# Kernel optimization log

Measured on AMD Instinct MI355X. Metric: run time of the kernel, lower is better.

Reference implementation:

```python
import jax, jax.numpy as jnp
import numpy as np

N = 100000   # nodes
E = 3200000  # random edges (before self-loops)
D = 20       # hidden width


def setup_inputs() -> dict:
    key = jax.random.key(0)
    k = jax.random.split(key, 8)
    return {
        "feat": jax.random.normal(k[0], (N, 1), jnp.float32),
        "W_start": jax.random.normal(k[1], (1, D), jnp.float32) * 0.5,
        "b_start": jnp.zeros((D,), jnp.float32),
        "W_mid": jax.random.normal(k[2], (18, D, D), jnp.float32) * (1.0 / np.sqrt(D)),
        "b_mid": jnp.zeros((18, D), jnp.float32),
        "W_final": jax.random.normal(k[3], (D, D), jnp.float32) * (1.0 / np.sqrt(D)),
        "b_final": jnp.zeros((D,), jnp.float32),
        "src": jax.random.randint(k[4], (E,), 0, N, jnp.int32),
        "dst": jax.random.randint(k[5], (E,), 0, N, jnp.int32),
    }


def reference(feat, W_start, b_start, W_mid, b_mid, W_final, b_final, src, dst):
    # dgl.add_self_loop
    loop = jnp.arange(N, dtype=src.dtype)
    src2 = jnp.concatenate([src, loop])
    dst2 = jnp.concatenate([dst, loop])

    ones = jnp.ones(src2.shape[0], jnp.float32)
    out_deg = jax.ops.segment_sum(ones, src2, num_segments=N)
    in_deg = jax.ops.segment_sum(ones, dst2, num_segments=N)
    # with self-loops degrees >= 1; clamp defensively like DGL
    dout = jnp.power(jnp.maximum(out_deg, 1.0), -0.5)  # [N]
    din = jnp.power(jnp.maximum(in_deg, 1.0), -0.5)    # [N]

    def conv(h, W, b):
        # GraphConv norm='both': D_out^{-1/2} on source, sum-aggregate, D_in^{-1/2} on dest
        hw = (h * dout[:, None]) @ W                   # [N, out]
        agg = jax.ops.segment_sum(hw[src2], dst2, num_segments=N)
        return agg * din[:, None] + b

    h = jax.nn.relu(conv(feat, W_start, b_start))

    def step(h, wb):
        W, b = wb
        return jax.nn.relu(conv(h, W, b)), None

    h, _ = jax.lax.scan(step, h, (W_mid, b_mid))
    h = conv(h, W_final, b_final)
    return h[None]  # unsqueeze(0) -> [1, N, D]
```

## Files before the change

kernel.cpp:

```cpp
#include <hip/hip_runtime.h>

#define DH    20
#define BKSC  10
#define BKC   1024
#define MAXKC 128
#define MAXNB 512
#define BKSF  8
#define BKF   256
#define ECAP  10240
#define CHUNK 8192


__global__ void zero_bhist2(int* __restrict__ bhist_d, int* __restrict__ bhist_s) {
    int i = threadIdx.x;
    if (i < MAXKC) { bhist_d[i] = 0; bhist_s[i] = 0; }
}

__global__ __launch_bounds__(256) void bucket_hist2(const int* __restrict__ src,
        const int* __restrict__ dst, int* __restrict__ pbh_d,
        int* __restrict__ pbh_s, int* __restrict__ bhist_d,
        int* __restrict__ bhist_s, int E, int K) {
    __shared__ int hd[MAXKC];
    __shared__ int hs[MAXKC];
    for (int i = threadIdx.x; i < K; i += blockDim.x) { hd[i] = 0; hs[i] = 0; }
    __syncthreads();
    int lo = blockIdx.x * CHUNK;
    int hi = lo + CHUNK; if (hi > E) hi = E;
    for (int e = lo + (int)threadIdx.x; e < hi; e += 256) {
        atomicAdd(&hd[__builtin_nontemporal_load(&dst[e]) >> BKSC], 1);
        atomicAdd(&hs[__builtin_nontemporal_load(&src[e]) >> BKSC], 1);
    }
    __syncthreads();
    for (int i = threadIdx.x; i < K; i += blockDim.x) {
        pbh_d[blockIdx.x * MAXKC + i] = hd[i];
        pbh_s[blockIdx.x * MAXKC + i] = hs[i];
        if (hd[i]) atomicAdd(&bhist_d[i], hd[i]);
        if (hs[i]) atomicAdd(&bhist_s[i], hs[i]);
    }
}

__global__ __launch_bounds__(128) void bucket_scan2(
        const int* __restrict__ bhist_d, int* __restrict__ bbase_d,
        int* __restrict__ bcursor_d, const int* __restrict__ bhist_s,
        int* __restrict__ bbase_s, int* __restrict__ bcursor_s, int K) {
    __shared__ int a[MAXKC];
    __shared__ int b[MAXKC];
    int t = threadIdx.x;
    int vd = (t < K) ? bhist_d[t] : 0;
    int vs = (t < K) ? bhist_s[t] : 0;
    a[t] = vd; b[t] = vs;
    __syncthreads();
    for (int off = 1; off < 128; off <<= 1) {
        int x = (t >= off) ? a[t - off] : 0;
        int y = (t >= off) ? b[t - off] : 0;
        __syncthreads();
        a[t] += x; b[t] += y;
        __syncthreads();
    }
    if (t < K) {
        int ed = a[t] - vd, es = b[t] - vs;
        bbase_d[t] = ed; bcursor_d[t] = ed;
        bbase_s[t] = es; bcursor_s[t] = es;
    }
    if (t == K - 1) { bbase_d[K] = a[t]; bbase_s[K] = b[t]; }
}

__global__ __launch_bounds__(256) void bucket_place(const int* __restrict__ src,
        const int* __restrict__ dst, const int* __restrict__ pbh_d,
        const int* __restrict__ pbh_s, int* __restrict__ bcursor_d,
        int* __restrict__ bcursor_s, int* __restrict__ pairs,
        int* __restrict__ ssort, int E, int K) {
    __shared__ int cd[MAXKC];
    __shared__ int cs[MAXKC];
    for (int i = threadIdx.x; i < K; i += blockDim.x) {
        int nd = pbh_d[blockIdx.x * MAXKC + i];
        int ns = pbh_s[blockIdx.x * MAXKC + i];
        cd[i] = nd ? atomicAdd(&bcursor_d[i], nd) : 0;
        cs[i] = ns ? atomicAdd(&bcursor_s[i], ns) : 0;
    }
    __syncthreads();
    int lo = blockIdx.x * CHUNK;
    int hi = lo + CHUNK; if (hi > E) hi = E;
    for (int e = lo + (int)threadIdx.x; e < hi; e += 256) {
        int d = __builtin_nontemporal_load(&dst[e]);
        int s = __builtin_nontemporal_load(&src[e]);
        int pd = atomicAdd(&cd[d >> BKSC], 1);
        pairs[pd] = (s << BKSC) | (d & (BKC - 1));
        int ps = atomicAdd(&cs[s >> BKSC], 1);
        ssort[ps] = s & (BKC - 1);
    }
}

__global__ __launch_bounds__(256) void bucket_outdeg(const int* __restrict__ bbase_s,
        const int* __restrict__ ssort, double* __restrict__ dout, int n_nodes) {
    __shared__ int h[BKC];
    int k = blockIdx.x;
    int t = threadIdx.x;
    int nbase = k << BKSC;
    int nrem = n_nodes - nbase; if (nrem > BKC) nrem = BKC;
    for (int i = t; i < BKC; i += 256) h[i] = 1;
    __syncthreads();
    int e0 = bbase_s[k], e1 = bbase_s[k + 1];
    for (int e = e0 + t; e < e1; e += 256)
        atomicAdd(&h[__builtin_nontemporal_load(&ssort[e])], 1);
    __syncthreads();
    for (int i = t; i < nrem; i += 256)
        dout[nbase + i] = 1.0 / sqrt((double)h[i]);
}

__global__ __launch_bounds__(256) void bucket_build(
        const int* __restrict__ bbase, const int* __restrict__ pairs,
        int* __restrict__ row_ptr, double* __restrict__ din,
        int* __restrict__ col, int n_nodes, int n_edges) {
    __shared__ int h[BKF];
    __shared__ int ts[BKF];
    __shared__ int red[256];
    __shared__ int ecol[ECAP];
    int nwg = gridDim.x;
    int xcd = blockIdx.x & 7;
    int loc = blockIdx.x >> 3;
    int q = nwg >> 3, r = nwg & 7;
    int k = ((xcd < r) ? xcd * (q + 1) : r * (q + 1) + (xcd - r) * q) + loc;
    int kc = k >> 2;
    int f  = k & 3;
    int t = threadIdx.x;
    int nbase = k << BKSF;
    int nrem = n_nodes - nbase; if (nrem > BKF) nrem = BKF;
    h[t] = 0;
    __syncthreads();
    int e0 = bbase[kc], e1 = bbase[kc + 1];
    int before = 0;
    for (int e = e0 + t; e < e1; e += 256) {
        int pk = pairs[e];
        int dl = pk & (BKC - 1);
        int fe = dl >> BKSF;
        if (fe == f) atomicAdd(&h[dl & (BKF - 1)], 1);
        else if (fe < f) ++before;
    }
    red[t] = before;
    __syncthreads();
    for (int off = 128; off > 0; off >>= 1) {
        if (t < off) red[t] += red[t + off];
        __syncthreads();
    }
    int fbase = e0 + red[0];
    int c = h[t];
    ts[t] = c;
    __syncthreads();
    for (int off = 1; off < 256; off <<= 1) {
        int v = (t >= off) ? ts[t - off] : 0;
        __syncthreads();
        ts[t] += v;
        __syncthreads();
    }
    int lx = ts[t] - c;
    if (t < nrem) {
        row_ptr[nbase + t] = fbase + lx;
        din[nbase + t] = 1.0 / sqrt((double)(c + 1));
    }
    h[t] = lx;
    if (t == 0 && nbase + BKF >= n_nodes) row_ptr[n_nodes] = n_edges;
    __syncthreads();
    for (int e = e0 + t; e < e1; e += 256) {
        int pk = pairs[e];
        int dl = pk & (BKC - 1);
        if ((dl >> BKSF) == f) {
            int slot = atomicAdd(&h[dl & (BKF - 1)], 1);
            if (slot < ECAP) ecol[slot] = pk >> BKSC;
            else col[fbase + slot] = pk >> BKSC;
        }
    }
    __syncthreads();
    int cnt = ts[BKF - 1];
    int lim = cnt < ECAP ? cnt : ECAP;
    for (int i = t; i < lim; i += 256)
        col[fbase + i] = ecol[i];
}


__global__ void compute_x0(const float* __restrict__ feat, const double* __restrict__ dout,
                           double* __restrict__ x0, int n) {
    int i = blockIdx.x * blockDim.x + threadIdx.x;
    if (i < n) x0[i] = (double)feat[i] * dout[i];
}

__global__ __launch_bounds__(256) void layer_start(
        const double* __restrict__ x0, const int* __restrict__ row_ptr,
        const int* __restrict__ col, const double* __restrict__ din,
        const double* __restrict__ dout, const float* __restrict__ W,
        const float* __restrict__ b, float* __restrict__ xout, int n_nodes) {
    int n    = (blockIdx.x * blockDim.x + threadIdx.x) >> 6;
    int lane = threadIdx.x & 63;
    if (n >= n_nodes) return;
    double a = (lane == 0) ? x0[n] : 0.0;
    int e0 = row_ptr[n], e1 = row_ptr[n + 1];
    for (int e = e0 + lane; e < e1; e += 64)
        a += x0[__builtin_nontemporal_load(&col[e])];
#pragma unroll
    for (int off = 32; off > 0; off >>= 1)
        a += __shfl_xor(a, off, 64);
    if (lane < DH) {
        double v = a * din[n] * (double)W[lane] + (double)b[lane];
        float r = fmaxf((float)v, 0.0f);
        xout[(long)n * DH + lane] = (float)((double)r * dout[n]);
    }
}

__global__ __launch_bounds__(256) void transform(
        const float* __restrict__ h, const float* __restrict__ W,
        float* __restrict__ y, int n_nodes) {
    __shared__ float Wl[DH * DH];
    for (int i = threadIdx.x; i < DH * DH; i += blockDim.x) Wl[i] = W[i];
    __syncthreads();
    int n = blockIdx.x * blockDim.x + threadIdx.x;
    if (n >= n_nodes) return;
    const float4* h4 = (const float4*)(h + (size_t)n * DH);
    float4 a0 = h4[0], a1 = h4[1], a2 = h4[2], a3 = h4[3], a4 = h4[4];
    float hv[DH] = {a0.x, a0.y, a0.z, a0.w, a1.x, a1.y, a1.z, a1.w,
                    a2.x, a2.y, a2.z, a2.w, a3.x, a3.y, a3.z, a3.w,
                    a4.x, a4.y, a4.z, a4.w};
    double acc[DH];
#pragma unroll
    for (int j = 0; j < DH; ++j) acc[j] = 0.0;
#pragma unroll
    for (int k = 0; k < DH; ++k) {
        double hk = (double)hv[k];
#pragma unroll
        for (int j = 0; j < DH; ++j)
            acc[j] += hk * (double)Wl[k * DH + j];
    }
    float4* y4 = (float4*)(y + (size_t)n * DH);
    y4[0] = make_float4((float)acc[0],  (float)acc[1],  (float)acc[2],  (float)acc[3]);
    y4[1] = make_float4((float)acc[4],  (float)acc[5],  (float)acc[6],  (float)acc[7]);
    y4[2] = make_float4((float)acc[8],  (float)acc[9],  (float)acc[10], (float)acc[11]);
    y4[3] = make_float4((float)acc[12], (float)acc[13], (float)acc[14], (float)acc[15]);
    y4[4] = make_float4((float)acc[16], (float)acc[17], (float)acc[18], (float)acc[19]);
}

__global__ __launch_bounds__(256, 8) void gather_agg(
        const float* __restrict__ y, const int* __restrict__ row_ptr,
        const int* __restrict__ col, const double* __restrict__ din,
        const double* __restrict__ dout, const float* __restrict__ b,
        float* __restrict__ hout, int n_nodes, int mode) {
    int n    = (blockIdx.x * blockDim.x + threadIdx.x) >> 6;
    int lane = threadIdx.x & 63;
    if (n >= n_nodes) return;

    int ep = lane / 5;
    int jq = lane - ep * 5;
    const float4* __restrict__ y4 = (const float4*)y;

    int e0 = row_ptr[n], e1 = row_ptr[n + 1];

    int s0 = -1, s1 = -1, s2 = -1, s3 = -1;
    if (ep < 12) {
        int p = e0 + ep;
        if (p      < e1) s0 = __builtin_nontemporal_load(&col[p]);
        if (p + 12 < e1) s1 = __builtin_nontemporal_load(&col[p + 12]);
        if (p + 24 < e1) s2 = __builtin_nontemporal_load(&col[p + 24]);
        if (p + 36 < e1) s3 = __builtin_nontemporal_load(&col[p + 36]);
    }
    bool p0 = s0 >= 0, p1 = s1 >= 0, p2 = s2 >= 0, p3 = s3 >= 0;
    float4 v0 = y4[(p0 ? s0 : n) * 5 + jq];
    float4 v1 = y4[(p1 ? s1 : n) * 5 + jq];
    float4 v2 = y4[(p2 ? s2 : n) * 5 + jq];
    float4 v3 = y4[(p3 ? s3 : n) * 5 + jq];

    double g[4] = {0.0, 0.0, 0.0, 0.0};
    if (ep == 0) {
        float4 v = y4[n * 5 + jq];
        g[0] = (double)v.x; g[1] = (double)v.y; g[2] = (double)v.z; g[3] = (double)v.w;
    }
    if (p0) { g[0] += (double)v0.x; g[1] += (double)v0.y; g[2] += (double)v0.z; g[3] += (double)v0.w; }
    if (p1) { g[0] += (double)v1.x; g[1] += (double)v1.y; g[2] += (double)v1.z; g[3] += (double)v1.w; }
    if (p2) { g[0] += (double)v2.x; g[1] += (double)v2.y; g[2] += (double)v2.z; g[3] += (double)v2.w; }
    if (p3) { g[0] += (double)v3.x; g[1] += (double)v3.y; g[2] += (double)v3.z; g[3] += (double)v3.w; }

    if (e1 - e0 > 48) {
        if (ep < 12) {
            for (int e = e0 + 48 + ep; e < e1; e += 12) {
                int s = __builtin_nontemporal_load(&col[e]);
                float4 v = y4[s * 5 + jq];
                g[0] += (double)v.x; g[1] += (double)v.y;
                g[2] += (double)v.z; g[3] += (double)v.w;
            }
        }
    }

    float f0 = (float)g[0], f1 = (float)g[1], f2 = (float)g[2], f3 = (float)g[3];
#define FOLD(LIM, DELTA)                                                        \
    {                                                                           \
        int srcl = lane + DELTA; if (srcl > 63) srcl = lane;                    \
        float t0 = __shfl(f0, srcl, 64);                                        \
        float t1 = __shfl(f1, srcl, 64);                                        \
        float t2 = __shfl(f2, srcl, 64);                                        \
        float t3 = __shfl(f3, srcl, 64);                                        \
        if (ep < (LIM)) { f0 += t0; f1 += t1; f2 += t2; f3 += t3; }             \
    }
    FOLD(4, 40)
    FOLD(4, 20)
    FOLD(2, 10)
    FOLD(1, 5)
#undef FOLD

    if (lane < 5) {
        double dn = din[n];
        float4 bb = ((const float4*)b)[lane];
        double o0 = (double)f0 * dn + (double)bb.x;
        double o1 = (double)f1 * dn + (double)bb.y;
        double o2 = (double)f2 * dn + (double)bb.z;
        double o3 = (double)f3 * dn + (double)bb.w;
        float4 w;
        if (mode == 0) {
            double dd = dout[n];
            w.x = (float)((double)fmaxf((float)o0, 0.0f) * dd);
            w.y = (float)((double)fmaxf((float)o1, 0.0f) * dd);
            w.z = (float)((double)fmaxf((float)o2, 0.0f) * dd);
            w.w = (float)((double)fmaxf((float)o3, 0.0f) * dd);
        } else {
            w.x = (float)o0; w.y = (float)o1; w.z = (float)o2; w.w = (float)o3;
        }
        ((float4*)(hout + (size_t)n * DH))[lane] = w;
    }
}


static inline size_t align256(size_t x) { return (x + 255) & ~(size_t)255; }

extern "C" void kernel_launch(void* const* d_in, const int* in_sizes, int n_in,
                              void* d_out, int out_size, void* d_ws, size_t ws_size,
                              hipStream_t stream) {
    const float* feat    = (const float*)d_in[0];
    const float* W_start = (const float*)d_in[1];
    const float* b_start = (const float*)d_in[2];
    const float* W_mid   = (const float*)d_in[3];
    const float* b_mid   = (const float*)d_in[4];
    const float* W_final = (const float*)d_in[5];
    const float* b_final = (const float*)d_in[6];
    const int*   src     = (const int*)d_in[7];
    const int*   dst     = (const int*)d_in[8];

    const int N = in_sizes[0];
    const int E = in_sizes[7];
    const int L = in_sizes[3] / (DH * DH);
    const int KC = (N + BKC - 1) / BKC;
    const int KF = (N + BKF - 1) / BKF;
    const int NB = (E + CHUNK - 1) / CHUNK;

    char* p = (char*)d_ws;
    double* dout_d = (double*)p; p += align256(sizeof(double) * N);
    double* din_d  = (double*)p; p += align256(sizeof(double) * N);
    double* x0     = (double*)p; p += align256(sizeof(double) * N);
    int* row_ptr   = (int*)p;    p += align256(sizeof(int) * (N + 1));
    int* bhist_d   = (int*)p;    p += align256(sizeof(int) * (MAXKC + 1));
    int* bhist_s   = (int*)p;    p += align256(sizeof(int) * (MAXKC + 1));
    int* bbase_d   = (int*)p;    p += align256(sizeof(int) * (MAXKC + 1));
    int* bbase_s   = (int*)p;    p += align256(sizeof(int) * (MAXKC + 1));
    int* bcursor_d = (int*)p;    p += align256(sizeof(int) * (MAXKC + 1));
    int* bcursor_s = (int*)p;    p += align256(sizeof(int) * (MAXKC + 1));
    int* pbh_d     = (int*)p;    p += align256(sizeof(int) * MAXNB * MAXKC);
    int* pbh_s     = (int*)p;    p += align256(sizeof(int) * MAXNB * MAXKC);
    int* col       = (int*)p;    p += align256(sizeof(int) * E);
    float* hbuf    = (float*)p;  p += align256(sizeof(float) * N * DH);
    float* ybuf    = (float*)p;  p += align256(sizeof(float) * N * DH);
    int* pairs = (int*)hbuf;
    int* ssort = col;

    const int BT = 256;
    int grid_n  = (N + BT - 1) / BT;
    int grid_nw = (N + 3) / 4;

    zero_bhist2<<<1, MAXKC, 0, stream>>>(bhist_d, bhist_s);
    bucket_hist2<<<NB, BT, 0, stream>>>(src, dst, pbh_d, pbh_s,
                                        bhist_d, bhist_s, E, KC);
    bucket_scan2<<<1, 128, 0, stream>>>(bhist_d, bbase_d, bcursor_d,
                                        bhist_s, bbase_s, bcursor_s, KC);
    bucket_place<<<NB, BT, 0, stream>>>(src, dst, pbh_d, pbh_s,
                                        bcursor_d, bcursor_s, pairs, ssort, E, KC);
    bucket_outdeg<<<KC, BT, 0, stream>>>(bbase_s, ssort, dout_d, N);
    bucket_build<<<KF, BT, 0, stream>>>(bbase_d, pairs, row_ptr, din_d, col, N, E);

    compute_x0<<<grid_n, BT, 0, stream>>>(feat, dout_d, x0, N);
    layer_start<<<grid_nw, BT, 0, stream>>>(x0, row_ptr, col, din_d, dout_d,
                                            W_start, b_start, hbuf, N);

    for (int l = 0; l < L; ++l) {
        transform<<<grid_n, BT, 0, stream>>>(hbuf, W_mid + (size_t)l * DH * DH, ybuf, N);
        gather_agg<<<grid_nw, BT, 0, stream>>>(ybuf, row_ptr, col, din_d, dout_d,
                                               b_mid + (size_t)l * DH, hbuf, N, 0);
    }

    transform<<<grid_n, BT, 0, stream>>>(hbuf, W_final, ybuf, N);
    gather_agg<<<grid_nw, BT, 0, stream>>>(ybuf, row_ptr, col, din_d, dout_d,
                                           b_final, (float*)d_out, N, 1);
}
```

Before: 1.631 ms.

## Split transformed features into 8- and 12-column arrays gathered separately

The transform now writes its 20-wide output into two separate arrays, one holding columns 0-7 and one holding columns 8-19. Two specialised gather kernels then aggregate each array in its own pass. The aim is a smaller random-access working set per pass, so neighbour feature rows are more likely to stay in cache. In exchange, the CSR column indices are read twice and twice as many gather kernels are launched per layer.

```diff
diff --git a/kernel.cpp b/kernel.cpp
--- a/kernel.cpp
+++ b/kernel.cpp
@@ -208,7 +208,7 @@
 
 __global__ __launch_bounds__(256) void transform(
         const float* __restrict__ h, const float* __restrict__ W,
-        float* __restrict__ y, int n_nodes) {
+        float4* __restrict__ y8, float4* __restrict__ y12, int n_nodes) {
     __shared__ float Wl[DH * DH];
     for (int i = threadIdx.x; i < DH * DH; i += blockDim.x) Wl[i] = W[i];
     __syncthreads();
@@ -229,83 +229,72 @@
         for (int j = 0; j < DH; ++j)
             acc[j] += hk * (double)Wl[k * DH + j];
     }
-    float4* y4 = (float4*)(y + (size_t)n * DH);
-    y4[0] = make_float4((float)acc[0],  (float)acc[1],  (float)acc[2],  (float)acc[3]);
-    y4[1] = make_float4((float)acc[4],  (float)acc[5],  (float)acc[6],  (float)acc[7]);
-    y4[2] = make_float4((float)acc[8],  (float)acc[9],  (float)acc[10], (float)acc[11]);
-    y4[3] = make_float4((float)acc[12], (float)acc[13], (float)acc[14], (float)acc[15]);
-    y4[4] = make_float4((float)acc[16], (float)acc[17], (float)acc[18], (float)acc[19]);
-}
-
-__global__ __launch_bounds__(256, 8) void gather_agg(
-        const float* __restrict__ y, const int* __restrict__ row_ptr,
+    y8[n * 2 + 0]  = make_float4((float)acc[0],  (float)acc[1],  (float)acc[2],  (float)acc[3]);
+    y8[n * 2 + 1]  = make_float4((float)acc[4],  (float)acc[5],  (float)acc[6],  (float)acc[7]);
+    y12[n * 3 + 0] = make_float4((float)acc[8],  (float)acc[9],  (float)acc[10], (float)acc[11]);
+    y12[n * 3 + 1] = make_float4((float)acc[12], (float)acc[13], (float)acc[14], (float)acc[15]);
+    y12[n * 3 + 2] = make_float4((float)acc[16], (float)acc[17], (float)acc[18], (float)acc[19]);
+}
+
+__global__ __launch_bounds__(256, 8) void gather8(
+        const float4* __restrict__ y8, const int* __restrict__ row_ptr,
         const int* __restrict__ col, const double* __restrict__ din,
         const double* __restrict__ dout, const float* __restrict__ b,
         float* __restrict__ hout, int n_nodes, int mode) {
     int n    = (blockIdx.x * blockDim.x + threadIdx.x) >> 6;
     int lane = threadIdx.x & 63;
     if (n >= n_nodes) return;
-
-    int ep = lane / 5;
-    int jq = lane - ep * 5;
-    const float4* __restrict__ y4 = (const float4*)y;
+    int jq = lane & 1;
+    int ep = lane >> 1;
 
     int e0 = row_ptr[n], e1 = row_ptr[n + 1];
-
-    int s0 = -1, s1 = -1, s2 = -1, s3 = -1;
-    if (ep < 12) {
+    int s0 = -1, s1 = -1;
+    {
         int p = e0 + ep;
         if (p      < e1) s0 = __builtin_nontemporal_load(&col[p]);
-        if (p + 12 < e1) s1 = __builtin_nontemporal_load(&col[p + 12]);
-        if (p + 24 < e1) s2 = __builtin_nontemporal_load(&col[p + 24]);
-        if (p + 36 < e1) s3 = __builtin_nontemporal_load(&col[p + 36]);
-    }
-    bool p0 = s0 >= 0, p1 = s1 >= 0, p2 = s2 >= 0, p3 = s3 >= 0;
-    float4 v0 = y4[(p0 ? s0 : n) * 5 + jq];
-    float4 v1 = y4[(p1 ? s1 : n) * 5 + jq];
-    float4 v2 = y4[(p2 ? s2 : n) * 5 + jq];
-    float4 v3 = y4[(p3 ? s3 : n) * 5 + jq];
+        if (p + 32 < e1) s1 = __builtin_nontemporal_load(&col[p + 32]);
+    }
+    bool p0 = s0 >= 0, p1 = s1 >= 0;
+    float4 v0 = y8[(p0 ? s0 : n) * 2 + jq];
+    float4 v1 = y8[(p1 ? s1 : n) * 2 + jq];
 
     double g[4] = {0.0, 0.0, 0.0, 0.0};
     if (ep == 0) {
-        float4 v = y4[n * 5 + jq];
+        float4 v = y8[n * 2 + jq];
         g[0] = (double)v.x; g[1] = (double)v.y; g[2] = (double)v.z; g[3] = (double)v.w;
     }
     if (p0) { g[0] += (double)v0.x; g[1] += (double)v0.y; g[2] += (double)v0.z; g[3] += (double)v0.w; }
     if (p1) { g[0] += (double)v1.x; g[1] += (double)v1.y; g[2] += (double)v1.z; g[3] += (double)v1.w; }
-    if (p2) { g[0] += (double)v2.x; g[1] += (double)v2.y; g[2] += (double)v2.z; g[3] += (double)v2.w; }
-    if (p3) { g[0] += (double)v3.x; g[1] += (double)v3.y; g[2] += (double)v3.z; g[3] += (double)v3.w; }
-
-    if (e1 - e0 > 48) {
-        if (ep < 12) {
-            for (int e = e0 + 48 + ep; e < e1; e += 12) {
-                int s = __builtin_nontemporal_load(&col[e]);
-                float4 v = y4[s * 5 + jq];
-                g[0] += (double)v.x; g[1] += (double)v.y;
-                g[2] += (double)v.z; g[3] += (double)v.w;
-            }
+
+    if (e1 - e0 > 64) {
+        for (int e = e0 + 64 + ep; e < e1; e += 32) {
+            int s = __builtin_nontemporal_load(&col[e]);
+            float4 v = y8[s * 2 + jq];
+            g[0] += (double)v.x; g[1] += (double)v.y;
+            g[2] += (double)v.z; g[3] += (double)v.w;
         }
     }
 
     float f0 = (float)g[0], f1 = (float)g[1], f2 = (float)g[2], f3 = (float)g[3];
-#define FOLD(LIM, DELTA)                                                        \
+#define FOLD8(LIM, DL)                                                          \
     {                                                                           \
-        int srcl = lane + DELTA; if (srcl > 63) srcl = lane;                    \
+        int srcl = lane + DL; if (srcl > 63) srcl = lane;                       \
         float t0 = __shfl(f0, srcl, 64);                                        \
         float t1 = __shfl(f1, srcl, 64);                                        \
         float t2 = __shfl(f2, srcl, 64);                                        \
         float t3 = __shfl(f3, srcl, 64);                                        \
         if (ep < (LIM)) { f0 += t0; f1 += t1; f2 += t2; f3 += t3; }             \
     }
-    FOLD(4, 40)
-    FOLD(4, 20)
-    FOLD(2, 10)
-    FOLD(1, 5)
-#undef FOLD
-
-    if (lane < 5) {
+    FOLD8(16, 32)
+    FOLD8(8, 16)
+    FOLD8(4, 8)
+    FOLD8(2, 4)
+    FOLD8(1, 2)
+#undef FOLD8
+
+    if (lane < 2) {
         double dn = din[n];
-        float4 bb = ((const float4*)b)[lane];
+        float4 bb = ((const float4*)b)[jq];
         double o0 = (double)f0 * dn + (double)bb.x;
         double o1 = (double)f1 * dn + (double)bb.y;
         double o2 = (double)f2 * dn + (double)bb.z;
@@ -320,7 +309,89 @@
         } else {
             w.x = (float)o0; w.y = (float)o1; w.z = (float)o2; w.w = (float)o3;
         }
-        ((float4*)(hout + (size_t)n * DH))[lane] = w;
+        *(float4*)(hout + (size_t)n * DH + jq * 4) = w;
+    }
+}
+
+__global__ __launch_bounds__(256, 8) void gather12(
+        const float4* __restrict__ y12, const int* __restrict__ row_ptr,
+        const int* __restrict__ col, const double* __restrict__ din,
+        const double* __restrict__ dout, const float* __restrict__ b,
+        float* __restrict__ hout, int n_nodes, int mode) {
+    int n    = (blockIdx.x * blockDim.x + threadIdx.x) >> 6;
+    int lane = threadIdx.x & 63;
+    if (n >= n_nodes) return;
+    int ep = lane / 3;
+    int jq = lane - ep * 3;
+
+    int e0 = row_ptr[n], e1 = row_ptr[n + 1];
+    int s0 = -1, s1 = -1, s2 = -1;
+    if (ep < 21) {
+        int p = e0 + ep;
+        if (p      < e1) s0 = __builtin_nontemporal_load(&col[p]);
+        if (p + 21 < e1) s1 = __builtin_nontemporal_load(&col[p + 21]);
+        if (p + 42 < e1) s2 = __builtin_nontemporal_load(&col[p + 42]);
+    }
+    bool p0 = s0 >= 0, p1 = s1 >= 0, p2 = s2 >= 0;
+    float4 v0 = y12[(p0 ? s0 : n) * 3 + jq];
+    float4 v1 = y12[(p1 ? s1 : n) * 3 + jq];
+    float4 v2 = y12[(p2 ? s2 : n) * 3 + jq];
+
+    double g[4] = {0.0, 0.0, 0.0, 0.0};
+    if (ep == 0) {
+        float4 v = y12[n * 3 + jq];
+        g[0] = (double)v.x; g[1] = (double)v.y; g[2] = (double)v.z; g[3] = (double)v.w;
+    }
+    if (p0) { g[0] += (double)v0.x; g[1] += (double)v0.y; g[2] += (double)v0.z; g[3] += (double)v0.w; }
+    if (p1) { g[0] += (double)v1.x; g[1] += (double)v1.y; g[2] += (double)v1.z; g[3] += (double)v1.w; }
+    if (p2) { g[0] += (double)v2.x; g[1] += (double)v2.y; g[2] += (double)v2.z; g[3] += (double)v2.w; }
+
+    if (e1 - e0 > 63) {
+        if (ep < 21) {
+            for (int e = e0 + 63 + ep; e < e1; e += 21) {
+                int s = __builtin_nontemporal_load(&col[e]);
+                float4 v = y12[s * 3 + jq];
+                g[0] += (double)v.x; g[1] += (double)v.y;
+                g[2] += (double)v.z; g[3] += (double)v.w;
+            }
+        }
+    }
+
+    float f0 = (float)g[0], f1 = (float)g[1], f2 = (float)g[2], f3 = (float)g[3];
+#define FOLD12(LIM, DL)                                                         \
+    {                                                                           \
+        int srcl = lane + DL; if (srcl > 63) srcl = lane;                       \
+        float t0 = __shfl(f0, srcl, 64);                                        \
+        float t1 = __shfl(f1, srcl, 64);                                        \
+        float t2 = __shfl(f2, srcl, 64);                                        \
+        float t3 = __shfl(f3, srcl, 64);                                        \
+        if (ep < (LIM)) { f0 += t0; f1 += t1; f2 += t2; f3 += t3; }             \
+    }
+    FOLD12(5, 48)
+    FOLD12(8, 24)
+    FOLD12(4, 12)
+    FOLD12(2, 6)
+    FOLD12(1, 3)
+#undef FOLD12
+
+    if (lane < 3) {
+        double dn = din[n];
+        float4 bb = ((const float4*)(b + 8))[jq];
+        double o0 = (double)f0 * dn + (double)bb.x;
+        double o1 = (double)f1 * dn + (double)bb.y;
+        double o2 = (double)f2 * dn + (double)bb.z;
+        double o3 = (double)f3 * dn + (double)bb.w;
+        float4 w;
+        if (mode == 0) {
+            double dd = dout[n];
+            w.x = (float)((double)fmaxf((float)o0, 0.0f) * dd);
+            w.y = (float)((double)fmaxf((float)o1, 0.0f) * dd);
+            w.z = (float)((double)fmaxf((float)o2, 0.0f) * dd);
+            w.w = (float)((double)fmaxf((float)o3, 0.0f) * dd);
+        } else {
+            w.x = (float)o0; w.y = (float)o1; w.z = (float)o2; w.w = (float)o3;
+        }
+        *(float4*)(hout + (size_t)n * DH + 8 + jq * 4) = w;
     }
 }
 
@@ -362,7 +433,8 @@
     int* pbh_s     = (int*)p;    p += align256(sizeof(int) * MAXNB * MAXKC);
     int* col       = (int*)p;    p += align256(sizeof(int) * E);
     float* hbuf    = (float*)p;  p += align256(sizeof(float) * N * DH);
-    float* ybuf    = (float*)p;  p += align256(sizeof(float) * N * DH);
+    float4* y8     = (float4*)p; p += align256(sizeof(float4) * N * 2);
+    float4* y12    = (float4*)p; p += align256(sizeof(float4) * N * 3);
     int* pairs = (int*)hbuf;
     int* ssort = col;
 
@@ -385,12 +457,17 @@
                                             W_start, b_start, hbuf, N);
 
     for (int l = 0; l < L; ++l) {
-        transform<<<grid_n, BT, 0, stream>>>(hbuf, W_mid + (size_t)l * DH * DH, ybuf, N);
-        gather_agg<<<grid_nw, BT, 0, stream>>>(ybuf, row_ptr, col, din_d, dout_d,
-                                               b_mid + (size_t)l * DH, hbuf, N, 0);
-    }
-
-    transform<<<grid_n, BT, 0, stream>>>(hbuf, W_final, ybuf, N);
-    gather_agg<<<grid_nw, BT, 0, stream>>>(ybuf, row_ptr, col, din_d, dout_d,
-                                           b_final, (float*)d_out, N, 1);
-}
+        transform<<<grid_n, BT, 0, stream>>>(hbuf, W_mid + (size_t)l * DH * DH,
+                                             y8, y12, N);
+        gather8<<<grid_nw, BT, 0, stream>>>(y8, row_ptr, col, din_d, dout_d,
+                                            b_mid + (size_t)l * DH, hbuf, N, 0);
+        gather12<<<grid_nw, BT, 0, stream>>>(y12, row_ptr, col, din_d, dout_d,
+                                             b_mid + (size_t)l * DH, hbuf, N, 0);
+    }
+
+    transform<<<grid_n, BT, 0, stream>>>(hbuf, W_final, y8, y12, N);
+    gather8<<<grid_nw, BT, 0, stream>>>(y8, row_ptr, col, din_d, dout_d,
+                                        b_final, (float*)d_out, N, 1);
+    gather12<<<grid_nw, BT, 0, stream>>>(y12, row_ptr, col, din_d, dout_d,
+                                         b_final, (float*)d_out, N, 1);
+}
```

Result: slower. 2.295 ms (+40.7%).
